# Kernel tuning notes

Hardware: AMD Instinct MI355X
Metric: run time of the kernel (lower is better)

Reference implementation:

```python
import jax, jax.numpy as jnp
import numpy as np

NEG_SLOPE = 0.2  # PyG GATConv default negative_slope


def _gat_layer(x, src, dst, W_src, W_dst, att_src, att_dst, bias, num_nodes):
    """Single-head GATConv (concat=True, heads=1, add_self_loops=False)."""
    h_src = x @ W_src                      # [N, C]
    h_dst = x @ W_dst                      # [N, C]
    a_src = h_src @ att_src                # [N]
    a_dst = h_dst @ att_dst                # [N]
    # per-edge attention logits: message j -> i uses a_src[j] + a_dst[i]
    e = jax.nn.leaky_relu(a_src[src] + a_dst[dst], NEG_SLOPE)  # [E]
    # numerically stable softmax over incoming edges of each destination
    m = jax.ops.segment_max(e, dst, num_segments=num_nodes)    # [N]
    ee = jnp.exp(e - m[dst])                                   # [E]
    denom = jax.ops.segment_sum(ee, dst, num_segments=num_nodes)  # [N]
    alpha = ee / denom[dst]                                    # [E]
    # attention-weighted scatter-add of source messages
    out = jax.ops.segment_sum(h_src[src] * alpha[:, None], dst,
                              num_segments=num_nodes)          # [N, C]
    return out + bias


def setup_inputs() -> dict:
    key = jax.random.key(0)
    ks = jax.random.split(key, 12)
    N, E, F_IN, HID, OUT = 100000, 1600000, 128, 128, 64
    inp = {
        "x": jax.random.normal(ks[0], (N, F_IN), dtype=jnp.float32),
        "edge_index": jax.random.randint(ks[1], (2, E), 0, N, dtype=jnp.int64
                                         if jax.config.jax_enable_x64 else jnp.int32),
        "W_src1": jax.random.normal(ks[2], (F_IN, HID), dtype=jnp.float32) / np.sqrt(F_IN),
        "W_dst1": jax.random.normal(ks[3], (F_IN, HID), dtype=jnp.float32) / np.sqrt(F_IN),
        "att_src1": jax.random.normal(ks[4], (HID,), dtype=jnp.float32) / np.sqrt(HID),
        "att_dst1": jax.random.normal(ks[5], (HID,), dtype=jnp.float32) / np.sqrt(HID),
        "b1": jnp.zeros((HID,), dtype=jnp.float32),
        "W_src2": jax.random.normal(ks[6], (HID, OUT), dtype=jnp.float32) / np.sqrt(HID),
        "W_dst2": jax.random.normal(ks[7], (HID, OUT), dtype=jnp.float32) / np.sqrt(HID),
        "att_src2": jax.random.normal(ks[8], (OUT,), dtype=jnp.float32) / np.sqrt(OUT),
        "att_dst2": jax.random.normal(ks[9], (OUT,), dtype=jnp.float32) / np.sqrt(OUT),
        "b2": jnp.zeros((OUT,), dtype=jnp.float32),
    }
    return inp


def reference(x, edge_index, W_src1, W_dst1, att_src1, att_dst1, b1,
              W_src2, W_dst2, att_src2, att_dst2, b2):
    N = x.shape[0]
    src, dst = edge_index[0], edge_index[1]
    h = _gat_layer(x, src, dst, W_src1, W_dst1, att_src1, att_dst1, b1, N)
    h = jax.nn.relu(h)
    out = _gat_layer(h, src, dst, W_src2, W_dst2, att_src2, att_dst2, b2, N)
    return out
```

## Files before the change

### kernel.cpp

```cpp
#include <hip/hip_runtime.h>

#define F_IN 128
#define NEG_SLOPE 0.2f
#define SCAN_CHUNK 2048

typedef __attribute__((ext_vector_type(8))) short bf16x8;
typedef __attribute__((ext_vector_type(4))) float f32x4;

__device__ inline unsigned short f2bf(float f) {
    unsigned int u = __float_as_uint(f);
    unsigned int r = (u + 0x7fffu + ((u >> 16) & 1u)) >> 16;
    return (unsigned short)r;
}
__device__ inline float bf2f(unsigned short h) { return __uint_as_float((unsigned int)h << 16); }
__device__ inline float bflo(unsigned int u) { return __uint_as_float(u << 16); }
__device__ inline float bfhi(unsigned int u) { return __uint_as_float(u & 0xffff0000u); }

__device__ inline int bswiz(int n, int k) {
    int ct = n >> 4, rlo = n & 15, kk = k >> 5, q = (k >> 3) & 3, j = k & 7;
    return (((ct * 4 + kk) * 64 + q * 16 + rlo) << 3) + j;
}

__global__ void k_prep(const float* __restrict__ Ws1, const float* __restrict__ Wd1,
                       const float* __restrict__ as1, const float* __restrict__ ad1,
                       const float* __restrict__ Ws2, const float* __restrict__ Wd2,
                       const float* __restrict__ as2, const float* __restrict__ ad2,
                       float* __restrict__ vecs, int* __restrict__ cnt,
                       unsigned short* __restrict__ w1hi, unsigned short* __restrict__ w1lo,
                       unsigned short* __restrict__ w2hi, unsigned short* __restrict__ w2lo,
                       int N) {
    int bid = blockIdx.x, tid = threadIdx.x;
    int i = bid * 256 + tid;
    if (i < N) cnt[i] = 0;
    if (bid == 0 && tid < 128) {
        int f = tid;
        float s1 = 0.f, d1 = 0.f, s2 = 0.f, d2 = 0.f;
        for (int c = 0; c < 128; ++c) {
            s1 += Ws1[f * 128 + c] * as1[c];
            d1 += Wd1[f * 128 + c] * ad1[c];
        }
        for (int c = 0; c < 64; ++c) {
            s2 += Ws2[f * 64 + c] * as2[c];
            d2 += Wd2[f * 64 + c] * ad2[c];
        }
        vecs[f] = s1; vecs[128 + f] = d1; vecs[256 + f] = s2; vecs[384 + f] = d2;
    } else if (bid >= 1 && bid < 65) {
        int idx = (bid - 1) * 256 + tid;
        int n = idx >> 7, k = idx & 127;
        float w = Ws1[k * 128 + n];
        unsigned short h = f2bf(w);
        int si = bswiz(n, k);
        w1hi[si] = h;
        w1lo[si] = f2bf(w - bf2f(h));
    } else if (bid >= 65 && bid < 97) {
        int idx = (bid - 65) * 256 + tid;
        int n = idx >> 7, k = idx & 127;
        float w = Ws2[k * 64 + n];
        unsigned short h = f2bf(w);
        int si = bswiz(n, k);
        w2hi[si] = h;
        w2lo[si] = f2bf(w - bf2f(h));
    }
}

__global__ void k_hist(const int* __restrict__ dsts, int* __restrict__ cnt,
                       int* __restrict__ rank, int E) {
    int e0 = (blockIdx.x * 256 + threadIdx.x) * 4;
    if (e0 + 4 <= E) {
        int4 d4 = *(const int4*)(dsts + e0);
        int4 r4;
        r4.x = atomicAdd(&cnt[d4.x], 1);
        r4.y = atomicAdd(&cnt[d4.y], 1);
        r4.z = atomicAdd(&cnt[d4.z], 1);
        r4.w = atomicAdd(&cnt[d4.w], 1);
        *(int4*)(rank + e0) = r4;
    } else {
        for (int e = e0; e < E; ++e) rank[e] = atomicAdd(&cnt[dsts[e]], 1);
    }
}

__global__ void k_blocksum(const int* __restrict__ cnt, int* __restrict__ bsum, int N) {
    __shared__ int sh[256];
    int t = threadIdx.x;
    long long base = (long long)blockIdx.x * SCAN_CHUNK + (long long)t * 8;
    int s = 0;
    #pragma unroll
    for (int k = 0; k < 8; ++k) {
        long long i = base + k;
        if (i < N) s += cnt[i];
    }
    sh[t] = s;
    __syncthreads();
    for (int off = 128; off; off >>= 1) {
        if (t < off) sh[t] += sh[t + off];
        __syncthreads();
    }
    if (t == 0) bsum[blockIdx.x] = sh[0];
}

__global__ void k_scan_chunks(const int* __restrict__ cnt, const int* __restrict__ bsum,
                              int* __restrict__ rowptr, int nb, int N) {
    __shared__ int sh[256];
    int t = threadIdx.x;
    int bid = blockIdx.x;
    int pre = 0;
    for (int b = 0; b < bid; ++b) pre += bsum[b];
    long long base = (long long)bid * SCAN_CHUNK + (long long)t * 8;
    int loc[8];
    int s = 0;
    #pragma unroll
    for (int k = 0; k < 8; ++k) {
        long long i = base + k;
        int v = (i < N) ? cnt[i] : 0;
        loc[k] = s;
        s += v;
    }
    sh[t] = s;
    __syncthreads();
    for (int off = 1; off < 256; off <<= 1) {
        int tmp = (t >= off) ? sh[t - off] : 0;
        __syncthreads();
        sh[t] += tmp;
        __syncthreads();
    }
    int toff = pre + sh[t] - s;
    #pragma unroll
    for (int k = 0; k < 8; ++k) {
        long long i = base + k;
        if (i < N) rowptr[i] = toff + loc[k];
    }
    if (bid == nb - 1 && t == 255) rowptr[N] = pre + sh[255];
}

__global__ void k_place(const int* __restrict__ srcs, const int* __restrict__ dsts,
                        const int* __restrict__ rowptr, const int* __restrict__ rank,
                        int* __restrict__ perm_src, int E) {
    int e0 = (blockIdx.x * 256 + threadIdx.x) * 4;
    if (e0 + 4 <= E) {
        int4 s4 = *(const int4*)(srcs + e0);
        int4 d4 = *(const int4*)(dsts + e0);
        int4 r4 = *(const int4*)(rank + e0);
        int p0 = rowptr[d4.x], p1 = rowptr[d4.y];
        int p2 = rowptr[d4.z], p3 = rowptr[d4.w];
        perm_src[p0 + r4.x] = s4.x;
        perm_src[p1 + r4.y] = s4.y;
        perm_src[p2 + r4.z] = s4.z;
        perm_src[p3 + r4.w] = s4.w;
    } else {
        for (int e = e0; e < E; ++e)
            perm_src[rowptr[dsts[e]] + rank[e]] = srcs[e];
    }
}

template <int COLS, bool ABF16>
__launch_bounds__(256)
__global__ void k_gemm_mfma(const void* __restrict__ Xv,
                            const unsigned short* __restrict__ Bh,
                            const unsigned short* __restrict__ Bl,
                            const float* __restrict__ vecs_s,
                            const float* __restrict__ vecs_d,
                            unsigned short* __restrict__ H,
                            float* __restrict__ a_s, float* __restrict__ a_d, int N) {
    int tid = threadIdx.x;
    int wave = tid >> 6, lane = tid & 63;
    int q = lane >> 4, rlo = lane & 15;
    long long wrow0 = (long long)blockIdx.x * 128 + wave * 32;

    bf16x8 Ahi[2][4], Alo[2][4];
    #pragma unroll
    for (int rt = 0; rt < 2; ++rt) {
        long long r = wrow0 + rt * 16 + rlo;
        long long rr = (r < N) ? r : (long long)(N - 1);
        float ps = 0.f, pd = 0.f;
        #pragma unroll
        for (int kk = 0; kk < 4; ++kk) {
            int k0 = kk * 32 + q * 8;
            float xv[8];
            if constexpr (ABF16) {
                const unsigned short* Xu = (const unsigned short*)Xv;
                bf16x8 av = *(const bf16x8*)(Xu + rr * 128 + k0);
                Ahi[rt][kk] = av;
                #pragma unroll
                for (int j = 0; j < 8; ++j) xv[j] = bf2f((unsigned short)av[j]);
            } else {
                const float* Xf = (const float*)Xv;
                float4 x0 = *(const float4*)(Xf + rr * 128 + k0);
                float4 x1 = *(const float4*)(Xf + rr * 128 + k0 + 4);
                xv[0] = x0.x; xv[1] = x0.y; xv[2] = x0.z; xv[3] = x0.w;
                xv[4] = x1.x; xv[5] = x1.y; xv[6] = x1.z; xv[7] = x1.w;
                bf16x8 ah, al;
                #pragma unroll
                for (int j = 0; j < 8; ++j) {
                    unsigned short h = f2bf(xv[j]);
                    ah[j] = (short)h;
                    al[j] = (short)f2bf(xv[j] - bf2f(h));
                }
                Ahi[rt][kk] = ah; Alo[rt][kk] = al;
            }
            float4 vs0 = *(const float4*)(vecs_s + k0);
            float4 vs1 = *(const float4*)(vecs_s + k0 + 4);
            float4 vd0 = *(const float4*)(vecs_d + k0);
            float4 vd1 = *(const float4*)(vecs_d + k0 + 4);
            ps += xv[0] * vs0.x + xv[1] * vs0.y + xv[2] * vs0.z + xv[3] * vs0.w
                + xv[4] * vs1.x + xv[5] * vs1.y + xv[6] * vs1.z + xv[7] * vs1.w;
            pd += xv[0] * vd0.x + xv[1] * vd0.y + xv[2] * vd0.z + xv[3] * vd0.w
                + xv[4] * vd1.x + xv[5] * vd1.y + xv[6] * vd1.z + xv[7] * vd1.w;
        }
        ps += __shfl_xor(ps, 16); ps += __shfl_xor(ps, 32);
        pd += __shfl_xor(pd, 16); pd += __shfl_xor(pd, 32);
        if (q == 0 && r < N) { a_s[r] = ps; a_d[r] = pd; }
    }

    const bf16x8* Bh8 = (const bf16x8*)Bh;
    const bf16x8* Bl8 = (const bf16x8*)Bl;
    #pragma unroll 1
    for (int ct = 0; ct < COLS / 16; ++ct) {
        bf16x8 bh[4], bl[4];
        #pragma unroll
        for (int kk = 0; kk < 4; ++kk) {
            bh[kk] = Bh8[(ct * 4 + kk) * 64 + lane];
            bl[kk] = Bl8[(ct * 4 + kk) * 64 + lane];
        }
        f32x4 acc0 = {0.f, 0.f, 0.f, 0.f};
        f32x4 acc1 = {0.f, 0.f, 0.f, 0.f};
        #pragma unroll
        for (int kk = 0; kk < 4; ++kk) {
            acc0 = __builtin_amdgcn_mfma_f32_16x16x32_bf16(Ahi[0][kk], bh[kk], acc0, 0, 0, 0);
            acc1 = __builtin_amdgcn_mfma_f32_16x16x32_bf16(Ahi[1][kk], bh[kk], acc1, 0, 0, 0);
            if constexpr (!ABF16) {
                acc0 = __builtin_amdgcn_mfma_f32_16x16x32_bf16(Alo[0][kk], bh[kk], acc0, 0, 0, 0);
                acc1 = __builtin_amdgcn_mfma_f32_16x16x32_bf16(Alo[1][kk], bh[kk], acc1, 0, 0, 0);
            }
            acc0 = __builtin_amdgcn_mfma_f32_16x16x32_bf16(Ahi[0][kk], bl[kk], acc0, 0, 0, 0);
            acc1 = __builtin_amdgcn_mfma_f32_16x16x32_bf16(Ahi[1][kk], bl[kk], acc1, 0, 0, 0);
        }
        #pragma unroll
        for (int i2 = 0; i2 < 4; ++i2) {
            long long o0 = wrow0 + q * 4 + i2;
            long long o1 = wrow0 + 16 + q * 4 + i2;
            if (o0 < N) H[o0 * COLS + ct * 16 + rlo] = f2bf(acc0[i2]);
            if (o1 < N) H[o1 * COLS + ct * 16 + rlo] = f2bf(acc1[i2]);
        }
    }
}

__launch_bounds__(256)
__global__ void k_agg128(const int* __restrict__ rowptr, const int* __restrict__ perm,
                         const float* __restrict__ a_s, const float* __restrict__ a_d,
                         const unsigned short* __restrict__ H, const float* __restrict__ bias,
                         unsigned short* __restrict__ out_bf, int N) {
    int wave = (int)(((long long)blockIdx.x * 256 + threadIdx.x) >> 6);
    int lane = threadIdx.x & 63;
    if (wave >= N) return;
    int beg = __builtin_amdgcn_readfirstlane(rowptr[wave]);
    int end = __builtin_amdgcn_readfirstlane(rowptr[wave + 1]);
    float ad = __uint_as_float(__builtin_amdgcn_readfirstlane(__float_as_uint(a_d[wave])));

    const unsigned int* H32 = (const unsigned int*)H;
    float acc0 = 0.f, acc1 = 0.f, wsum = 0.f;
    int i = beg;
    for (; i + 8 <= end; i += 8) {
        int s[8];
        unsigned int v[8];
        #pragma unroll
        for (int j = 0; j < 8; ++j)
            s[j] = __builtin_amdgcn_readfirstlane(perm[i + j]);
        #pragma unroll
        for (int j = 0; j < 8; ++j)
            v[j] = H32[(long long)s[j] * 64 + lane];
        #pragma unroll
        for (int j = 0; j < 8; ++j) {
            float t = a_s[s[j]] + ad;
            t = t > 0.f ? t : NEG_SLOPE * t;
            float w = __expf(t);
            acc0 += w * bflo(v[j]);
            acc1 += w * bfhi(v[j]);
            wsum += w;
        }
    }
    for (; i < end; ++i) {
        int s = __builtin_amdgcn_readfirstlane(perm[i]);
        unsigned int v = H32[(long long)s * 64 + lane];
        float t = a_s[s] + ad;
        t = t > 0.f ? t : NEG_SLOPE * t;
        float w = __expf(t);
        acc0 += w * bflo(v); acc1 += w * bfhi(v);
        wsum += w;
    }
    float inv = (wsum > 0.f) ? __fdividef(1.f, wsum) : 0.f;
    float o0 = fmaxf(acc0 * inv + bias[2 * lane], 0.f);
    float o1 = fmaxf(acc1 * inv + bias[2 * lane + 1], 0.f);
    unsigned int pk = (unsigned int)f2bf(o0) | ((unsigned int)f2bf(o1) << 16);
    ((unsigned int*)out_bf)[(long long)wave * 64 + lane] = pk;
}

__launch_bounds__(256)
__global__ void k_agg64(const int* __restrict__ rowptr, const int* __restrict__ perm,
                        const float* __restrict__ a_s, const float* __restrict__ a_d,
                        const unsigned short* __restrict__ H, const float* __restrict__ bias,
                        float* __restrict__ out, int N) {
    int wave = (int)(((long long)blockIdx.x * 256 + threadIdx.x) >> 6);
    int lane = threadIdx.x & 63;
    if (wave >= N) return;
    int c = lane & 31, h = lane >> 5;
    int beg = __builtin_amdgcn_readfirstlane(rowptr[wave]);
    int end = __builtin_amdgcn_readfirstlane(rowptr[wave + 1]);
    float ad = __uint_as_float(__builtin_amdgcn_readfirstlane(__float_as_uint(a_d[wave])));

    const unsigned int* H32 = (const unsigned int*)H;
    float acc0 = 0.f, acc1 = 0.f, wsum = 0.f;
    int base = beg;
    for (; base + 16 <= end; base += 16) {
        int s[8];
        unsigned int v[8];
        #pragma unroll
        for (int j = 0; j < 8; ++j)
            s[j] = perm[base + h + 2 * j];
        #pragma unroll
        for (int j = 0; j < 8; ++j)
            v[j] = H32[(long long)s[j] * 32 + c];
        #pragma unroll
        for (int j = 0; j < 8; ++j) {
            float t = a_s[s[j]] + ad;
            t = t > 0.f ? t : NEG_SLOPE * t;
            float w = __expf(t);
            acc0 += w * bflo(v[j]);
            acc1 += w * bfhi(v[j]);
            wsum += w;
        }
    }
    for (; base + 8 <= end; base += 8) {
        int s[4];
        unsigned int v[4];
        #pragma unroll
        for (int j = 0; j < 4; ++j)
            s[j] = perm[base + h + 2 * j];
        #pragma unroll
        for (int j = 0; j < 4; ++j)
            v[j] = H32[(long long)s[j] * 32 + c];
        #pragma unroll
        for (int j = 0; j < 4; ++j) {
            float t = a_s[s[j]] + ad;
            t = t > 0.f ? t : NEG_SLOPE * t;
            float w = __expf(t);
            acc0 += w * bflo(v[j]);
            acc1 += w * bfhi(v[j]);
            wsum += w;
        }
    }
    for (int i = base + h; i < end; i += 2) {
        int s = perm[i];
        unsigned int v = H32[(long long)s * 32 + c];
        float t = a_s[s] + ad;
        t = t > 0.f ? t : NEG_SLOPE * t;
        float w = __expf(t);
        acc0 += w * bflo(v); acc1 += w * bfhi(v);
        wsum += w;
    }
    acc0 += __shfl_xor(acc0, 32);
    acc1 += __shfl_xor(acc1, 32);
    wsum += __shfl_xor(wsum, 32);
    if (h == 0) {
        float inv = (wsum > 0.f) ? __fdividef(1.f, wsum) : 0.f;
        float2 o;
        o.x = acc0 * inv + bias[2 * c];
        o.y = acc1 * inv + bias[2 * c + 1];
        *(float2*)(out + (long long)wave * 64 + 2 * c) = o;
    }
}

extern "C" void kernel_launch(void* const* d_in, const int* in_sizes, int n_in,
                              void* d_out, int out_size, void* d_ws, size_t ws_size,
                              hipStream_t stream) {
    const float* x   = (const float*)d_in[0];
    const int*   ei  = (const int*)d_in[1];
    const float* Ws1 = (const float*)d_in[2];
    const float* Wd1 = (const float*)d_in[3];
    const float* as1 = (const float*)d_in[4];
    const float* ad1 = (const float*)d_in[5];
    const float* b1  = (const float*)d_in[6];
    const float* Ws2 = (const float*)d_in[7];
    const float* Wd2 = (const float*)d_in[8];
    const float* as2 = (const float*)d_in[9];
    const float* ad2 = (const float*)d_in[10];
    const float* b2  = (const float*)d_in[11];
    float* out = (float*)d_out;

    const int N = in_sizes[0] / F_IN;
    const int E = in_sizes[1] / 2;
    const int* srcs = ei;
    const int* dsts = ei + E;

    unsigned short* hbuf = (unsigned short*)d_ws;
    unsigned short* x2bf = hbuf + (size_t)N * 128;
    int*   perm   = (int*)(x2bf + (size_t)N * 128);
    float* a_s1   = (float*)(perm + E);
    float* a_d1   = a_s1 + N;
    float* a_s2   = a_d1 + N;
    float* a_d2   = a_s2 + N;
    int*   cnt    = (int*)(a_d2 + N);
    int*   rowptr = cnt + N;
    int*   bsum   = rowptr + N + 4;
    unsigned short* w1hi = (unsigned short*)(bsum + 64);
    unsigned short* w1lo = w1hi + 16384;
    unsigned short* w2hi = w1lo + 16384;
    unsigned short* w2lo = w2hi + 8192;
    float* vecs   = (float*)(w2lo + 8192);
    int*   rank   = (int*)x2bf;

    const int nb = (N + SCAN_CHUNK - 1) / SCAN_CHUNK;

    k_prep<<<(N + 255) / 256, 256, 0, stream>>>(Ws1, Wd1, as1, ad1, Ws2, Wd2,
                                                as2, ad2, vecs, cnt,
                                                w1hi, w1lo, w2hi, w2lo, N);
    k_hist<<<(E / 4 + 255) / 256, 256, 0, stream>>>(dsts, cnt, rank, E);
    k_blocksum<<<nb, 256, 0, stream>>>(cnt, bsum, N);
    k_scan_chunks<<<nb, 256, 0, stream>>>(cnt, bsum, rowptr, nb, N);
    k_place<<<(E / 4 + 255) / 256, 256, 0, stream>>>(srcs, dsts, rowptr, rank, perm, E);

    k_gemm_mfma<128, false><<<(N + 127) / 128, 256, 0, stream>>>(
        x, w1hi, w1lo, vecs, vecs + 128, hbuf, a_s1, a_d1, N);
    k_agg128<<<(N + 3) / 4, 256, 0, stream>>>(
        rowptr, perm, a_s1, a_d1, hbuf, b1, x2bf, N);

    k_gemm_mfma<64, true><<<(N + 127) / 128, 256, 0, stream>>>(
        x2bf, w2hi, w2lo, vecs + 256, vecs + 384, hbuf, a_s2, a_d2, N);
    k_agg64<<<(N + 3) / 4, 256, 0, stream>>>(
        rowptr, perm, a_s2, a_d2, hbuf, b2, out, N);
}
```

Measured before the change: 377.7 us.

## Replace global-atomic CSR build with two-level LDS bucketed radix sort

The CSR construction (histogram with global atomics, scan, scatter) is replaced by a two-pass bucket sort. Edges are first binned by dst>>8 using shared-memory histograms per 4096-edge chunk, then a scan over the bucket-by-chunk table and a scatter of (dst,src) pairs. A per-bucket kernel then builds rowptr and perm with LDS atomics. This removes 1.6M contended global atomics and the random rank/rowptr reads, at the cost of an extra pass over a pair buffer and a larger scan table.

```diff
diff --git a/kernel.cpp b/kernel.cpp
--- a/kernel.cpp
+++ b/kernel.cpp
@@ -3,6 +3,7 @@
 #define F_IN 128
 #define NEG_SLOPE 0.2f
 #define SCAN_CHUNK 2048
+#define CH 4096
 
 typedef __attribute__((ext_vector_type(8))) short bf16x8;
 typedef __attribute__((ext_vector_type(4))) float f32x4;
@@ -25,13 +26,10 @@
                        const float* __restrict__ as1, const float* __restrict__ ad1,
                        const float* __restrict__ Ws2, const float* __restrict__ Wd2,
                        const float* __restrict__ as2, const float* __restrict__ ad2,
-                       float* __restrict__ vecs, int* __restrict__ cnt,
+                       float* __restrict__ vecs,
                        unsigned short* __restrict__ w1hi, unsigned short* __restrict__ w1lo,
-                       unsigned short* __restrict__ w2hi, unsigned short* __restrict__ w2lo,
-                       int N) {
+                       unsigned short* __restrict__ w2hi, unsigned short* __restrict__ w2lo) {
     int bid = blockIdx.x, tid = threadIdx.x;
-    int i = bid * 256 + tid;
-    if (i < N) cnt[i] = 0;
     if (bid == 0 && tid < 128) {
         int f = tid;
         float s1 = 0.f, d1 = 0.f, s2 = 0.f, d2 = 0.f;
@@ -63,23 +61,24 @@
     }
 }
 
-__global__ void k_hist(const int* __restrict__ dsts, int* __restrict__ cnt,
-                       int* __restrict__ rank, int E) {
-    int e0 = (blockIdx.x * 256 + threadIdx.x) * 4;
-    if (e0 + 4 <= E) {
-        int4 d4 = *(const int4*)(dsts + e0);
-        int4 r4;
-        r4.x = atomicAdd(&cnt[d4.x], 1);
-        r4.y = atomicAdd(&cnt[d4.y], 1);
-        r4.z = atomicAdd(&cnt[d4.z], 1);
-        r4.w = atomicAdd(&cnt[d4.w], 1);
-        *(int4*)(rank + e0) = r4;
-    } else {
-        for (int e = e0; e < E; ++e) rank[e] = atomicAdd(&cnt[dsts[e]], 1);
-    }
-}
-
-__global__ void k_blocksum(const int* __restrict__ cnt, int* __restrict__ bsum, int N) {
+
+__global__ void k_bhist(const int* __restrict__ dsts, int* __restrict__ table,
+                        int E, int NB, int nblk) {
+    __shared__ int bins[512];
+    int t = threadIdx.x, blk = blockIdx.x;
+    for (int j = t; j < NB; j += 256) bins[j] = 0;
+    __syncthreads();
+    int base = blk * CH;
+    #pragma unroll
+    for (int k = 0; k < CH / 256; ++k) {
+        int idx = base + k * 256 + t;
+        if (idx < E) atomicAdd(&bins[dsts[idx] >> 8], 1);
+    }
+    __syncthreads();
+    for (int j = t; j < NB; j += 256) table[(long long)j * nblk + blk] = bins[j];
+}
+
+__global__ void k_blocksum2(const int* __restrict__ in, int* __restrict__ bsum, int M) {
     __shared__ int sh[256];
     int t = threadIdx.x;
     long long base = (long long)blockIdx.x * SCAN_CHUNK + (long long)t * 8;
@@ -87,7 +86,7 @@
     #pragma unroll
     for (int k = 0; k < 8; ++k) {
         long long i = base + k;
-        if (i < N) s += cnt[i];
+        if (i < M) s += in[i];
     }
     sh[t] = s;
     __syncthreads();
@@ -98,11 +97,10 @@
     if (t == 0) bsum[blockIdx.x] = sh[0];
 }
 
-__global__ void k_scan_chunks(const int* __restrict__ cnt, const int* __restrict__ bsum,
-                              int* __restrict__ rowptr, int nb, int N) {
+__global__ void k_scan2(const int* __restrict__ in, const int* __restrict__ bsum,
+                        int* __restrict__ out, int M) {
     __shared__ int sh[256];
-    int t = threadIdx.x;
-    int bid = blockIdx.x;
+    int t = threadIdx.x, bid = blockIdx.x;
     int pre = 0;
     for (int b = 0; b < bid; ++b) pre += bsum[b];
     long long base = (long long)bid * SCAN_CHUNK + (long long)t * 8;
@@ -111,7 +109,7 @@
     #pragma unroll
     for (int k = 0; k < 8; ++k) {
         long long i = base + k;
-        int v = (i < N) ? cnt[i] : 0;
+        int v = (i < M) ? in[i] : 0;
         loc[k] = s;
         s += v;
     }
@@ -127,29 +125,66 @@
     #pragma unroll
     for (int k = 0; k < 8; ++k) {
         long long i = base + k;
-        if (i < N) rowptr[i] = toff + loc[k];
-    }
-    if (bid == nb - 1 && t == 255) rowptr[N] = pre + sh[255];
-}
-
-__global__ void k_place(const int* __restrict__ srcs, const int* __restrict__ dsts,
-                        const int* __restrict__ rowptr, const int* __restrict__ rank,
-                        int* __restrict__ perm_src, int E) {
-    int e0 = (blockIdx.x * 256 + threadIdx.x) * 4;
-    if (e0 + 4 <= E) {
-        int4 s4 = *(const int4*)(srcs + e0);
-        int4 d4 = *(const int4*)(dsts + e0);
-        int4 r4 = *(const int4*)(rank + e0);
-        int p0 = rowptr[d4.x], p1 = rowptr[d4.y];
-        int p2 = rowptr[d4.z], p3 = rowptr[d4.w];
-        perm_src[p0 + r4.x] = s4.x;
-        perm_src[p1 + r4.y] = s4.y;
-        perm_src[p2 + r4.z] = s4.z;
-        perm_src[p3 + r4.w] = s4.w;
-    } else {
-        for (int e = e0; e < E; ++e)
-            perm_src[rowptr[dsts[e]] + rank[e]] = srcs[e];
-    }
+        if (i < M) out[i] = toff + loc[k];
+    }
+}
+
+__global__ void k_bscat(const int* __restrict__ srcs, const int* __restrict__ dsts,
+                        const int* __restrict__ tscan, int2* __restrict__ pairA,
+                        int E, int NB, int nblk) {
+    __shared__ int offs[512];
+    int t = threadIdx.x, blk = blockIdx.x;
+    for (int j = t; j < NB; j += 256) offs[j] = tscan[(long long)j * nblk + blk];
+    __syncthreads();
+    int base = blk * CH;
+    #pragma unroll
+    for (int k = 0; k < CH / 256; ++k) {
+        int idx = base + k * 256 + t;
+        if (idx < E) {
+            int d = dsts[idx], s = srcs[idx];
+            int p = atomicAdd(&offs[d >> 8], 1);
+            int2 pr; pr.x = d; pr.y = s;
+            pairA[p] = pr;
+        }
+    }
+}
+
+__global__ void k_bfin(const int2* __restrict__ pairA, const int* __restrict__ tscan,
+                       int* __restrict__ perm, int* __restrict__ rowptr,
+                       int NB, int nblk, int N, int E) {
+    __shared__ int scnt[256];
+    __shared__ int sh[256];
+    __shared__ int sptr[256];
+    int t = threadIdx.x, b = blockIdx.x;
+    int beg = tscan[(long long)b * nblk];
+    int end = (b + 1 < NB) ? tscan[(long long)(b + 1) * nblk] : E;
+    scnt[t] = 0;
+    __syncthreads();
+    for (int i = beg + t; i < end; i += 256) {
+        int2 p = pairA[i];
+        atomicAdd(&scnt[p.x & 255], 1);
+    }
+    __syncthreads();
+    int c = scnt[t];
+    sh[t] = c;
+    __syncthreads();
+    for (int off = 1; off < 256; off <<= 1) {
+        int tmp = (t >= off) ? sh[t - off] : 0;
+        __syncthreads();
+        sh[t] += tmp;
+        __syncthreads();
+    }
+    int excl = sh[t] - c;
+    int node = (b << 8) + t;
+    if (node < N) rowptr[node] = beg + excl;
+    sptr[t] = beg + excl;
+    __syncthreads();
+    for (int i = beg + t; i < end; i += 256) {
+        int2 p = pairA[i];
+        int pos = atomicAdd(&sptr[p.x & 255], 1);
+        perm[pos] = p.y;
+    }
+    if (b == NB - 1 && t == 0) rowptr[N] = E;
 }
 
 template <int COLS, bool ABF16>
@@ -391,6 +426,11 @@
     const int* srcs = ei;
     const int* dsts = ei + E;
 
+    const int nblk = (E + CH - 1) / CH;
+    const int NB   = (N + 255) >> 8;
+    const int M    = NB * nblk;
+    const int nb2  = (M + SCAN_CHUNK - 1) / SCAN_CHUNK;
+
     unsigned short* hbuf = (unsigned short*)d_ws;
     unsigned short* x2bf = hbuf + (size_t)N * 128;
     int*   perm   = (int*)(x2bf + (size_t)N * 128);
@@ -398,25 +438,24 @@
     float* a_d1   = a_s1 + N;
     float* a_s2   = a_d1 + N;
     float* a_d2   = a_s2 + N;
-    int*   cnt    = (int*)(a_d2 + N);
-    int*   rowptr = cnt + N;
-    int*   bsum   = rowptr + N + 4;
-    unsigned short* w1hi = (unsigned short*)(bsum + 64);
+    int*   rowptr = (int*)(a_d2 + N);
+    int*   table  = rowptr + N + 4;
+    int*   tscan  = table + M + 4;
+    int*   bsum   = tscan + M + 4;
+    unsigned short* w1hi = (unsigned short*)(bsum + 128);
     unsigned short* w1lo = w1hi + 16384;
     unsigned short* w2hi = w1lo + 16384;
     unsigned short* w2lo = w2hi + 8192;
     float* vecs   = (float*)(w2lo + 8192);
-    int*   rank   = (int*)x2bf;
-
-    const int nb = (N + SCAN_CHUNK - 1) / SCAN_CHUNK;
-
-    k_prep<<<(N + 255) / 256, 256, 0, stream>>>(Ws1, Wd1, as1, ad1, Ws2, Wd2,
-                                                as2, ad2, vecs, cnt,
-                                                w1hi, w1lo, w2hi, w2lo, N);
-    k_hist<<<(E / 4 + 255) / 256, 256, 0, stream>>>(dsts, cnt, rank, E);
-    k_blocksum<<<nb, 256, 0, stream>>>(cnt, bsum, N);
-    k_scan_chunks<<<nb, 256, 0, stream>>>(cnt, bsum, rowptr, nb, N);
-    k_place<<<(E / 4 + 255) / 256, 256, 0, stream>>>(srcs, dsts, rowptr, rank, perm, E);
+    int2*  pairA  = (int2*)x2bf;
+
+    k_prep<<<97, 256, 0, stream>>>(Ws1, Wd1, as1, ad1, Ws2, Wd2, as2, ad2,
+                                   vecs, w1hi, w1lo, w2hi, w2lo);
+    k_bhist<<<nblk, 256, 0, stream>>>(dsts, table, E, NB, nblk);
+    k_blocksum2<<<nb2, 256, 0, stream>>>(table, bsum, M);
+    k_scan2<<<nb2, 256, 0, stream>>>(table, bsum, tscan, M);
+    k_bscat<<<nblk, 256, 0, stream>>>(srcs, dsts, tscan, pairA, E, NB, nblk);
+    k_bfin<<<NB, 256, 0, stream>>>(pairA, tscan, perm, rowptr, NB, nblk, N, E);
 
     k_gemm_mfma<128, false><<<(N + 127) / 128, 256, 0, stream>>>(
         x, w1hi, w1lo, vecs, vecs + 128, hbuf, a_s1, a_d1, N);
```

Result: faster. 323.3 us (-14.4%).
